# Kernel optimization log

Measured on AMD Instinct MI355X. Metric: run time of the kernel, lower is better.

The kernel has to match this reference:

```python
import jax, jax.numpy as jnp
import numpy as np

# physical constants (repo-level globals)
L1, L2, M1, M2 = 1.0, 1.0, 1.0, 1.0
G, K1 = 9.81, 0.5
A_E = 1.0   # energy-shaping stabilizer gain (a_M = 0 -> F_M term is exactly zero)
B_DAMP = 0.0
BATCH, HID = 500000, 64


def _V(q, W1, b1, W2, b2, W3, b3):
    # learned potential: [B,2] -> [B,1]
    h = jnp.tanh(q @ W1 + b1)
    h = jnp.tanh(h @ W2 + b2)
    return h @ W3 + b3


def _pot(q1, q2):
    return -G * (jnp.cos(q1 + q2) * L2 * M2 + jnp.cos(q1) * L1 * (M1 + M2)) + K1 * (0.5 * jnp.pi - q2) ** 2


def _inv_mass(q2):
    M_11 = 2 * jnp.cos(q2) * L1 * L2 * M2 + L2 ** 2 * M2 + L1 ** 2 * (M1 + M2)
    M_12 = L2 * (jnp.cos(q2) * L1 + L2) * M2
    M_22 = L2 ** 2 * M2
    DEN = M_11 * M_22 - M_12 ** 2
    return M_22 / DEN, -M_12 / DEN, M_11 / DEN


def setup_inputs() -> dict:
    key = jax.random.key(0)
    ks = jax.random.split(key, 8)
    s1 = 1.0 / np.sqrt(2.0)
    s2 = 1.0 / np.sqrt(HID)
    return {
        "x": jax.random.normal(ks[0], (BATCH, 4), jnp.float32),
        "t": jnp.zeros((1,), jnp.float32),
        "W1": jax.random.normal(ks[1], (2, HID), jnp.float32) * s1,
        "b1": jnp.zeros((HID,), jnp.float32),
        "W2": jax.random.normal(ks[2], (HID, HID), jnp.float32) * s2,
        "b2": jnp.zeros((HID,), jnp.float32),
        "W3": jax.random.normal(ks[3], (HID, 1), jnp.float32) * s2,
        "b3": jnp.zeros((1,), jnp.float32),
        "T_param": jnp.ones((1,), jnp.float32),
        "x0": jax.random.normal(ks[4], (4,), jnp.float32),
    }


def _forward(x, W1, b1, W2, b2, W3, b3, T_param, x0):
    q = x[:, :2]
    p = x[:, 2:]
    q1, q2 = q[:, 0], q[:, 1]
    p1, p2 = p[:, 0], p[:, 1]

    # u_energy_shaping = -dV/dq
    dVdq = jax.grad(lambda qq: _V(qq, W1, b1, W2, b2, W3, b3).sum())(q)
    u_es = -dVdq  # [B,2]

    # stabilizing control (a_M = 0 -> only F_E term)
    iM11, iM12, iM22 = _inv_mass(q2)
    quad = iM11 * p1 ** 2 + 2 * iM12 * p1 * p2 + iM22 * p2 ** 2  # p^T M^{-1} p
    kin = 0.5 * quad
    E = _pot(q1, q2) + kin + _V(q, W1, b1, W2, b2, W3, b3)[:, 0]

    # desired energy from x0 (set in _set_control_parameters)
    q0 = x0[:2][None, :]
    p0 = x0[2:]
    i011, i012, i022 = _inv_mass(q0[:, 1])
    kin0 = 0.5 * (i011 * p0[0] ** 2 + 2 * i012 * p0[0] * p0[1] + i022 * p0[1] ** 2)
    E_des = (_pot(q0[:, 0], q0[:, 1]) + kin0 + _V(q0, W1, b1, W2, b2, W3, b3)[:, 0])[0]

    pnorm = jnp.sqrt(quad)
    safe = jnp.where(pnorm > 0, pnorm, 1.0)
    p_hat = jnp.where((pnorm > 0)[:, None], p / safe[:, None], p)
    u_st = A_E * (E_des - E)[:, None] * p_hat

    u = u_es + u_st
    u1, u2 = u[:, 0], u[:, 1]

    # dynamics
    cq2, sq2 = jnp.cos(q2), jnp.sin(q2)
    DET = L1 ** 2 * L2 ** 2 * M2 ** 2 * (-(cq2 ** 2)) + L1 ** 2 * L2 ** 2 * M2 ** 2 + L1 ** 2 * L2 ** 2 * M1 * M2
    dq1dt = L2 ** 2 * M2 * p1 / DET - L2 * M2 * p2 * (L1 * cq2 + L2) / DET
    dq2dt = p2 * (2 * L2 * L1 * M2 * cq2 + L1 ** 2 * (M1 + M2) + L2 ** 2 * M2) / DET - L2 * M2 * p1 * (L1 * cq2 + L2) / DET
    dp1dt = -G * (jnp.sin(q1 + q2) * L2 * M2 + jnp.sin(q1) * L1 * (M1 + M2)) + u1 - B_DAMP * dq1dt
    denom = L1 ** 2 * L2 ** 2 * (M1 + sq2 ** 2 * M2) ** 2
    inner = (-(p2 ** 2) * sq2 * (cq2 * L1 + L2) * (cq2 * L2 * M2 + L1 * (M1 + M2))
             + 0.5 * p1 * p2 * sq2 * L2 * (4 * cq2 * L2 * M2 + L1 * (2 * M1 + (3 + jnp.cos(2 * q2)) * M2))
             + L2 ** 2 * (-cq2 * p1 ** 2 * sq2 * M2
                          + L1 ** 2 * (M1 + sq2 ** 2 * M2) ** 2 * (G * jnp.sin(q1 + q2) * L2 * M2 - K1 * (jnp.pi - 2 * q2))))
    dp2dt = -(inner / denom) + u2 - B_DAMP * dq2dt

    dxdt = jnp.stack([dq1dt, dq2dt, dp1dt, dp2dt], axis=1)
    return jnp.abs(T_param[0]) * dxdt


def reference(x, t, W1, b1, W2, b2, W3, b3, T_param, x0):
    # t is unused by the forward math (autonomous dynamics under ODE-solver interface)
    return _forward(x, W1, b1, W2, b2, W3, b3, T_param, x0)
```

## Files before the change

kernel.cpp:

```cpp
#include <hip/hip_runtime.h>
#include <math.h>

#define HID 64

typedef __attribute__((ext_vector_type(4))) float f32x4;
typedef __attribute__((ext_vector_type(8))) __bf16 bf16x8;
typedef __attribute__((ext_vector_type(4))) __bf16 bf16x4;

__device__ __forceinline__ float fast_tanh(float x) {
    float e = __expf(2.0f * x);
    return 1.0f - 2.0f * __builtin_amdgcn_rcpf(e + 1.0f);
}

__global__ void prep_kernel(const float* __restrict__ W1, const float* __restrict__ b1,
                            const float* __restrict__ W2, const float* __restrict__ b2,
                            const float* __restrict__ W3, const float* __restrict__ b3,
                            const float* __restrict__ x0, float* __restrict__ edes_out,
                            __bf16* __restrict__ W2bf, __bf16* __restrict__ W2Tbf) {
    int tid = threadIdx.x;
    for (int idx = tid; idx < HID * HID; idx += 256) {
        W2bf[idx] = (__bf16)W2[idx];
        int r = idx >> 6, c = idx & 63;
        W2Tbf[idx] = (__bf16)W2[c * HID + r];
    }
    if (tid < 64) {
        int j = tid;
        float q1 = x0[0], q2 = x0[1], p1 = x0[2], p2 = x0[3];
        float h1j = fast_tanh(fmaf(q1, W1[j], fmaf(q2, W1[HID + j], b1[j])));
        float z = b2[j];
#pragma unroll 1
        for (int i = 0; i < HID; i++) {
            float hi = __shfl(h1j, i, 64);
            z = fmaf(hi, W2[i * HID + j], z);
        }
        float h2 = fast_tanh(z);
        float v = h2 * W3[j];
#pragma unroll
        for (int off = 32; off; off >>= 1) v += __shfl_xor(v, off, 64);
        if (j == 0) {
            float V = v + b3[0];
            float s, c;
            __sincosf(q2, &s, &c);
            float DEN = 2.0f - c * c;
            float rDEN = __builtin_amdgcn_rcpf(DEN);
            float quad = (p1 * p1 - 2.0f * (c + 1.0f) * p1 * p2 + (2.0f * c + 3.0f) * p2 * p2) * rDEN;
            float kin = 0.5f * quad;
            float s1, c1;
            __sincosf(q1, &s1, &c1);
            float c12 = c1 * c - s1 * s;
            float dq = 1.57079632679489662f - q2;
            float pot = -9.81f * (c12 + 2.0f * c1) + 0.5f * dq * dq;
            edes_out[0] = pot + kin + V;
        }
    }
}

#define TANH8M(F, M, Q1v, Q2v)                                                                        \
    {                                                                                                 \
        float h;                                                                                      \
        h = fast_tanh(fmaf(Q1v, wa0.x, fmaf(Q2v, wb0.x, bb0.x))); F[0] = (__bf16)h; M[0] = (__bf16)fmaf(-h, h, 1.0f); \
        h = fast_tanh(fmaf(Q1v, wa0.y, fmaf(Q2v, wb0.y, bb0.y))); F[1] = (__bf16)h; M[1] = (__bf16)fmaf(-h, h, 1.0f); \
        h = fast_tanh(fmaf(Q1v, wa0.z, fmaf(Q2v, wb0.z, bb0.z))); F[2] = (__bf16)h; M[2] = (__bf16)fmaf(-h, h, 1.0f); \
        h = fast_tanh(fmaf(Q1v, wa0.w, fmaf(Q2v, wb0.w, bb0.w))); F[3] = (__bf16)h; M[3] = (__bf16)fmaf(-h, h, 1.0f); \
        h = fast_tanh(fmaf(Q1v, wa1.x, fmaf(Q2v, wb1.x, bb1.x))); F[4] = (__bf16)h; M[4] = (__bf16)fmaf(-h, h, 1.0f); \
        h = fast_tanh(fmaf(Q1v, wa1.y, fmaf(Q2v, wb1.y, bb1.y))); F[5] = (__bf16)h; M[5] = (__bf16)fmaf(-h, h, 1.0f); \
        h = fast_tanh(fmaf(Q1v, wa1.z, fmaf(Q2v, wb1.z, bb1.z))); F[6] = (__bf16)h; M[6] = (__bf16)fmaf(-h, h, 1.0f); \
        h = fast_tanh(fmaf(Q1v, wa1.w, fmaf(Q2v, wb1.w, bb1.w))); F[7] = (__bf16)h; M[7] = (__bf16)fmaf(-h, h, 1.0f); \
    }

#define L1HALF4(FA, FB, FC, FD, K0)                                         \
    do {                                                                    \
        const float4 wa0 = *(const float4*)(W1 + (K0));                     \
        const float4 wa1 = *(const float4*)(W1 + (K0) + 4);                 \
        const float4 wb0 = *(const float4*)(W1 + HID + (K0));               \
        const float4 wb1 = *(const float4*)(W1 + HID + (K0) + 4);           \
        const float4 bb0 = *(const float4*)(b1 + (K0));                     \
        const float4 bb1 = *(const float4*)(b1 + (K0) + 4);                 \
        bf16x8 mA, mB, mC, mD;                                              \
        TANH8M(FA, mA, q1A, q2A)                                            \
        TANH8M(FB, mB, q1B, q2B)                                            \
        TANH8M(FC, mC, q1C, q2C)                                            \
        TANH8M(FD, mD, q1D, q2D)                                            \
        const int mo = rowbase + ((K0) ^ swz);                              \
        *(bf16x8*)(mkA + mo) = mA;                                          \
        *(bf16x8*)(mkB + mo) = mB;                                          \
        *(bf16x8*)(mkC + mo) = mC;                                          \
        *(bf16x8*)(mkD + mo) = mD;                                          \
    } while (0)

#define MFMA __builtin_amdgcn_mfma_f32_16x16x32_bf16

#define H2ONE(Z, VP, GBUF, MT)                                                      \
    do {                                                                            \
        float h, g0_, g1_, g2_, g3_;                                                \
        h = fast_tanh(Z[0]); VP = fmaf(h, w3v.x, VP); g0_ = w3v.x * (1.0f - h * h); \
        h = fast_tanh(Z[1]); VP = fmaf(h, w3v.y, VP); g1_ = w3v.y * (1.0f - h * h); \
        h = fast_tanh(Z[2]); VP = fmaf(h, w3v.z, VP); g2_ = w3v.z * (1.0f - h * h); \
        h = fast_tanh(Z[3]); VP = fmaf(h, w3v.w, VP); g3_ = w3v.w * (1.0f - h * h); \
        bf16x4 gv = {(__bf16)g0_, (__bf16)g1_, (__bf16)g2_, (__bf16)g3_};           \
        *(bf16x4*)((GBUF) + rowbase + ((16 * (MT) + 4 * hi) ^ swz)) = gv;           \
    } while (0)

#define FWDMT(MT)                                                           \
    do {                                                                    \
        const float4 b2v = *(const float4*)(b2 + 16 * (MT) + 4 * hi);       \
        f32x4 zA = {b2v.x, b2v.y, b2v.z, b2v.w};                            \
        f32x4 zB = zA, zC = zA, zD = zA;                                    \
        const bf16x8 wf0 = *(const bf16x8*)(w2t + (MT) * 1024);             \
        zA = MFMA(wf0, a10A, zA, 0, 0, 0);                                  \
        zB = MFMA(wf0, a10B, zB, 0, 0, 0);                                  \
        zC = MFMA(wf0, a10C, zC, 0, 0, 0);                                  \
        zD = MFMA(wf0, a10D, zD, 0, 0, 0);                                  \
        const bf16x8 wf1 = *(const bf16x8*)(w2t + (MT) * 1024 + 32);        \
        zA = MFMA(wf1, a11A, zA, 0, 0, 0);                                  \
        zB = MFMA(wf1, a11B, zB, 0, 0, 0);                                  \
        zC = MFMA(wf1, a11C, zC, 0, 0, 0);                                  \
        zD = MFMA(wf1, a11D, zD, 0, 0, 0);                                  \
        const float4 w3v = *(const float4*)(W3 + 16 * (MT) + 4 * hi);       \
        H2ONE(zA, vpA, g2A, MT);                                            \
        H2ONE(zB, vpB, g2B, MT);                                            \
        H2ONE(zC, vpC, g2C, MT);                                            \
        H2ONE(zD, vpD, g2D, MT);                                            \
    } while (0)

#define DVONE(R, MK, MT, D1, D2)                                                              \
    do {                                                                                      \
        const bf16x4 mv = *(const bf16x4*)((MK) + rowbase + ((16 * (MT) + 4 * hi) ^ swz));    \
        float gi;                                                                             \
        gi = (float)mv[0] * R[0]; D1 = fmaf(w1av.x, gi, D1); D2 = fmaf(w1bv.x, gi, D2);       \
        gi = (float)mv[1] * R[1]; D1 = fmaf(w1av.y, gi, D1); D2 = fmaf(w1bv.y, gi, D2);       \
        gi = (float)mv[2] * R[2]; D1 = fmaf(w1av.z, gi, D1); D2 = fmaf(w1bv.z, gi, D2);       \
        gi = (float)mv[3] * R[3]; D1 = fmaf(w1av.w, gi, D1); D2 = fmaf(w1bv.w, gi, D2);       \
    } while (0)

#define BWDMT(MT)                                                           \
    do {                                                                    \
        f32x4 rA = {0.f, 0.f, 0.f, 0.f};                                    \
        f32x4 rB = rA, rC = rA, rD = rA;                                    \
        const bf16x8 wf0 = *(const bf16x8*)(w2b + (MT) * 1024);             \
        rA = MFMA(wf0, a20A, rA, 0, 0, 0);                                  \
        rB = MFMA(wf0, a20B, rB, 0, 0, 0);                                  \
        rC = MFMA(wf0, a20C, rC, 0, 0, 0);                                  \
        rD = MFMA(wf0, a20D, rD, 0, 0, 0);                                  \
        const bf16x8 wf1 = *(const bf16x8*)(w2b + (MT) * 1024 + 32);        \
        rA = MFMA(wf1, a21A, rA, 0, 0, 0);                                  \
        rB = MFMA(wf1, a21B, rB, 0, 0, 0);                                  \
        rC = MFMA(wf1, a21C, rC, 0, 0, 0);                                  \
        rD = MFMA(wf1, a21D, rD, 0, 0, 0);                                  \
        const float4 w1av = *(const float4*)(W1 + 16 * (MT) + 4 * hi);      \
        const float4 w1bv = *(const float4*)(W1 + HID + 16 * (MT) + 4 * hi);\
        DVONE(rA, mkA, MT, d1A, d2A);                                       \
        DVONE(rB, mkB, MT, d1B, d2B);                                       \
        DVONE(rC, mkC, MT, d1C, d2C);                                       \
        DVONE(rD, mkD, MT, d1D, d2D);                                       \
    } while (0)

#define RED2(V) V += __shfl_xor(V, 16, 64); V += __shfl_xor(V, 32, 64);

#define SEL4(A, B, C, D) ((hi == 0) ? (A) : (hi == 1) ? (B) : (hi == 2) ? (C) : (D))

__global__ __launch_bounds__(256, 2) void pend_kernel(
    const float4* __restrict__ x,
    const float* __restrict__ W1, const float* __restrict__ b1,
    const __bf16* __restrict__ W2bf, const __bf16* __restrict__ W2Tbf,
    const float* __restrict__ b2,
    const float* __restrict__ W3, const float* __restrict__ b3,
    const float* __restrict__ Tp, const float* __restrict__ edes_p,
    float4* __restrict__ out, int n)
{
    __shared__ __align__(16) __bf16 lds[4 * 8192];
    const int tid = threadIdx.x;
    const int w = tid >> 6, l = tid & 63;
    const int lo = l & 15, hi = l >> 4;
    __bf16* g2A = lds + w * 8192;
    __bf16* g2B = g2A + 1024;
    __bf16* g2C = g2B + 1024;
    __bf16* g2D = g2C + 1024;
    __bf16* mkA = g2D + 1024;
    __bf16* mkB = mkA + 1024;
    __bf16* mkC = mkB + 1024;
    __bf16* mkD = mkC + 1024;

    const float E_des = edes_p[0];
    const float Tabs = fabsf(Tp[0]);
    const float b3c = b3[0];

    const int base = blockIdx.x * 256 + w * 64;
    int eA = base + lo;       if (eA >= n) eA = n - 1;
    int eB = base + 16 + lo;  if (eB >= n) eB = n - 1;
    int eC = base + 32 + lo;  if (eC >= n) eC = n - 1;
    int eD = base + 48 + lo;  if (eD >= n) eD = n - 1;
    const float4 xvA = x[eA];
    const float4 xvB = x[eB];
    const float4 xvC = x[eC];
    const float4 xvD = x[eD];
    const float q1A = xvA.x, q2A = xvA.y, p1A = xvA.z, p2A = xvA.w;
    const float q1B = xvB.x, q2B = xvB.y, p1B = xvB.z, p2B = xvB.w;
    const float q1C = xvC.x, q2C = xvC.y, p1C = xvC.z, p2C = xvC.w;
    const float q1D = xvD.x, q2D = xvD.y, p1D = xvD.z, p2D = xvD.w;

    const int swz = (lo & 7) << 3;
    const int rowbase = lo * HID;

    bf16x8 a10A, a11A, a10B, a11B, a10C, a11C, a10D, a11D;
    L1HALF4(a10A, a10B, a10C, a10D, 8 * hi);
    L1HALF4(a11A, a11B, a11C, a11D, 32 + 8 * hi);

    const __bf16* w2t = W2Tbf + lo * HID + 8 * hi;
    const __bf16* w2b = W2bf  + lo * HID + 8 * hi;

    float vpA = 0.0f, vpB = 0.0f, vpC = 0.0f, vpD = 0.0f;
    FWDMT(0);
    FWDMT(1);
    FWDMT(2);
    FWDMT(3);

    const bf16x8 a20A = *(const bf16x8*)(g2A + rowbase + ((8 * hi) ^ swz));
    const bf16x8 a21A = *(const bf16x8*)(g2A + rowbase + ((32 + 8 * hi) ^ swz));
    const bf16x8 a20B = *(const bf16x8*)(g2B + rowbase + ((8 * hi) ^ swz));
    const bf16x8 a21B = *(const bf16x8*)(g2B + rowbase + ((32 + 8 * hi) ^ swz));
    const bf16x8 a20C = *(const bf16x8*)(g2C + rowbase + ((8 * hi) ^ swz));
    const bf16x8 a21C = *(const bf16x8*)(g2C + rowbase + ((32 + 8 * hi) ^ swz));
    const bf16x8 a20D = *(const bf16x8*)(g2D + rowbase + ((8 * hi) ^ swz));
    const bf16x8 a21D = *(const bf16x8*)(g2D + rowbase + ((32 + 8 * hi) ^ swz));

    float d1A = 0.f, d2A = 0.f, d1B = 0.f, d2B = 0.f;
    float d1C = 0.f, d2C = 0.f, d1D = 0.f, d2D = 0.f;
    BWDMT(0);
    BWDMT(1);
    BWDMT(2);
    BWDMT(3);

    RED2(vpA) RED2(vpB) RED2(vpC) RED2(vpD)
    RED2(d1A) RED2(d1B) RED2(d1C) RED2(d1D)
    RED2(d2A) RED2(d2B) RED2(d2C) RED2(d2D)

    const float V    = SEL4(vpA, vpB, vpC, vpD) + b3c;
    const float dVq1 = SEL4(d1A, d1B, d1C, d1D);
    const float dVq2 = SEL4(d2A, d2B, d2C, d2D);
    const float q1 = SEL4(q1A, q1B, q1C, q1D);
    const float q2 = SEL4(q2A, q2B, q2C, q2D);
    const float p1 = SEL4(p1A, p1B, p1C, p1D);
    const float p2 = SEL4(p2A, p2B, p2C, p2D);

    float s2q, c2q, s1q, c1q;
    __sincosf(q2, &s2q, &c2q);
    __sincosf(q1, &s1q, &c1q);
    const float s12 = s1q * c2q + c1q * s2q;
    const float c12 = c1q * c2q - s1q * s2q;

    const float cc = c2q, s = s2q;
    const float DEN = 2.0f - cc * cc;
    const float rDEN = __builtin_amdgcn_rcpf(DEN);
    const float cp1 = cc + 1.0f;

    const float quad = (p1 * p1 - 2.0f * cp1 * p1 * p2 + (2.0f * cc + 3.0f) * p2 * p2) * rDEN;
    const float kin = 0.5f * quad;
    const float dqa = 1.57079632679489662f - q2;
    const float pot = -9.81f * (c12 + 2.0f * c1q) + 0.5f * dqa * dqa;
    const float E = pot + kin + V;

    const float fac = (quad > 0.0f) ? __builtin_amdgcn_rsqf(quad) : 1.0f;
    const float coef = E_des - E;
    const float u1 = -dVq1 + coef * p1 * fac;
    const float u2 = -dVq2 + coef * p2 * fac;

    const float dq1dt = (p1 - cp1 * p2) * rDEN;
    const float dq2dt = ((2.0f * cc + 3.0f) * p2 - cp1 * p1) * rDEN;
    const float dp1dt = -9.81f * (s12 + 2.0f * s1q) + u1;

    const float inner = -p2 * p2 * s * cp1 * (cc + 2.0f)
                + p1 * p2 * s * (fmaf(cc, cc, fmaf(2.0f, cc, 2.0f)))
                - cc * p1 * p1 * s
                + DEN * DEN * (fmaf(9.81f, s12, -0.5f * (3.14159265358979324f - 2.0f * q2)));
    const float dp2dt = -(inner * rDEN * rDEN) + u2;

    const int row = base + l;
    if (row < n) {
        float4 o;
        o.x = Tabs * dq1dt;
        o.y = Tabs * dq2dt;
        o.z = Tabs * dp1dt;
        o.w = Tabs * dp2dt;
        out[row] = o;
    }
}

extern "C" void kernel_launch(void* const* d_in, const int* in_sizes, int n_in,
                              void* d_out, int out_size, void* d_ws, size_t ws_size,
                              hipStream_t stream) {
    const float* x  = (const float*)d_in[0];
    const float* W1 = (const float*)d_in[2];
    const float* b1 = (const float*)d_in[3];
    const float* W2 = (const float*)d_in[4];
    const float* b2 = (const float*)d_in[5];
    const float* W3 = (const float*)d_in[6];
    const float* b3 = (const float*)d_in[7];
    const float* Tp = (const float*)d_in[8];
    const float* x0 = (const float*)d_in[9];

    float* ws = (float*)d_ws;
    float* edes = ws;
    __bf16* W2bf  = (__bf16*)(ws + 16);
    __bf16* W2Tbf = W2bf + HID * HID;

    prep_kernel<<<1, 256, 0, stream>>>(W1, b1, W2, b2, W3, b3, x0, edes, W2bf, W2Tbf);

    int n = in_sizes[0] / 4;
    int blocks = (n + 255) / 256;
    pend_kernel<<<blocks, 256, 0, stream>>>((const float4*)x, W1, b1, W2bf, W2Tbf,
                                            b2, W3, b3, Tp, edes, (float4*)d_out, n);
}
```

Measured before the change: 44.48 us.

## Process sub-tiles in two sequential pairs to halve LDS and raise occupancy

Instead of running the MLP forward and backward for all four 16-row sub-tiles at once, each wave now handles two sub-tiles, then the other two, reusing half-sized LDS scratch buffers. This halves per-block LDS and cuts live registers, which lets launch bounds rise from 2 to 4 blocks per CU for more latency hiding. In exchange there is less instruction-level parallelism per wave and an added block-wide barrier between the two pairs. The per-wave buffers may only need a wave-level barrier.

Measured after the change: 103.7 us. 2.33x slower.

```diff
diff --git a/kernel.cpp b/kernel.cpp
--- a/kernel.cpp
+++ b/kernel.cpp
@@ -68,7 +68,7 @@
         h = fast_tanh(fmaf(Q1v, wa1.w, fmaf(Q2v, wb1.w, bb1.w))); F[7] = (__bf16)h; M[7] = (__bf16)fmaf(-h, h, 1.0f); \
     }
 
-#define L1HALF4(FA, FB, FC, FD, K0)                                         \
+#define L1HB(FX, FY, K0, Q1a_, Q2a_, Q1b_, Q2b_)                            \
     do {                                                                    \
         const float4 wa0 = *(const float4*)(W1 + (K0));                     \
         const float4 wa1 = *(const float4*)(W1 + (K0) + 4);                 \
@@ -76,16 +76,12 @@
         const float4 wb1 = *(const float4*)(W1 + HID + (K0) + 4);           \
         const float4 bb0 = *(const float4*)(b1 + (K0));                     \
         const float4 bb1 = *(const float4*)(b1 + (K0) + 4);                 \
-        bf16x8 mA, mB, mC, mD;                                              \
-        TANH8M(FA, mA, q1A, q2A)                                            \
-        TANH8M(FB, mB, q1B, q2B)                                            \
-        TANH8M(FC, mC, q1C, q2C)                                            \
-        TANH8M(FD, mD, q1D, q2D)                                            \
+        bf16x8 mX_, mY_;                                                    \
+        TANH8M(FX, mX_, Q1a_, Q2a_)                                         \
+        TANH8M(FY, mY_, Q1b_, Q2b_)                                         \
         const int mo = rowbase + ((K0) ^ swz);                              \
-        *(bf16x8*)(mkA + mo) = mA;                                          \
-        *(bf16x8*)(mkB + mo) = mB;                                          \
-        *(bf16x8*)(mkC + mo) = mC;                                          \
-        *(bf16x8*)(mkD + mo) = mD;                                          \
+        *(bf16x8*)(mk0 + mo) = mX_;                                         \
+        *(bf16x8*)(mk1 + mo) = mY_;                                         \
     } while (0)
 
 #define MFMA __builtin_amdgcn_mfma_f32_16x16x32_bf16
@@ -101,26 +97,20 @@
         *(bf16x4*)((GBUF) + rowbase + ((16 * (MT) + 4 * hi) ^ swz)) = gv;           \
     } while (0)
 
-#define FWDMT(MT)                                                           \
+#define FWDMT2(MT, VPa_, VPb_)                                              \
     do {                                                                    \
         const float4 b2v = *(const float4*)(b2 + 16 * (MT) + 4 * hi);       \
-        f32x4 zA = {b2v.x, b2v.y, b2v.z, b2v.w};                            \
-        f32x4 zB = zA, zC = zA, zD = zA;                                    \
+        f32x4 zX = {b2v.x, b2v.y, b2v.z, b2v.w};                            \
+        f32x4 zY = zX;                                                      \
         const bf16x8 wf0 = *(const bf16x8*)(w2t + (MT) * 1024);             \
-        zA = MFMA(wf0, a10A, zA, 0, 0, 0);                                  \
-        zB = MFMA(wf0, a10B, zB, 0, 0, 0);                                  \
-        zC = MFMA(wf0, a10C, zC, 0, 0, 0);                                  \
-        zD = MFMA(wf0, a10D, zD, 0, 0, 0);                                  \
+        zX = MFMA(wf0, a10X, zX, 0, 0, 0);                                  \
+        zY = MFMA(wf0, a10Y, zY, 0, 0, 0);                                  \
         const bf16x8 wf1 = *(const bf16x8*)(w2t + (MT) * 1024 + 32);        \
-        zA = MFMA(wf1, a11A, zA, 0, 0, 0);                                  \
-        zB = MFMA(wf1, a11B, zB, 0, 0, 0);                                  \
-        zC = MFMA(wf1, a11C, zC, 0, 0, 0);                                  \
-        zD = MFMA(wf1, a11D, zD, 0, 0, 0);                                  \
+        zX = MFMA(wf1, a11X, zX, 0, 0, 0);                                  \
+        zY = MFMA(wf1, a11Y, zY, 0, 0, 0);                                  \
         const float4 w3v = *(const float4*)(W3 + 16 * (MT) + 4 * hi);       \
-        H2ONE(zA, vpA, g2A, MT);                                            \
-        H2ONE(zB, vpB, g2B, MT);                                            \
-        H2ONE(zC, vpC, g2C, MT);                                            \
-        H2ONE(zD, vpD, g2D, MT);                                            \
+        H2ONE(zX, VPa_, g20, MT);                                           \
+        H2ONE(zY, VPb_, g21, MT);                                           \
     } while (0)
 
 #define DVONE(R, MK, MT, D1, D2)                                                              \
@@ -133,33 +123,46 @@
         gi = (float)mv[3] * R[3]; D1 = fmaf(w1av.w, gi, D1); D2 = fmaf(w1bv.w, gi, D2);       \
     } while (0)
 
-#define BWDMT(MT)                                                           \
+#define BWDMT2(MT, D1a_, D2a_, D1b_, D2b_)                                  \
     do {                                                                    \
-        f32x4 rA = {0.f, 0.f, 0.f, 0.f};                                    \
-        f32x4 rB = rA, rC = rA, rD = rA;                                    \
+        f32x4 rX = {0.f, 0.f, 0.f, 0.f};                                    \
+        f32x4 rY = rX;                                                      \
         const bf16x8 wf0 = *(const bf16x8*)(w2b + (MT) * 1024);             \
-        rA = MFMA(wf0, a20A, rA, 0, 0, 0);                                  \
-        rB = MFMA(wf0, a20B, rB, 0, 0, 0);                                  \
-        rC = MFMA(wf0, a20C, rC, 0, 0, 0);                                  \
-        rD = MFMA(wf0, a20D, rD, 0, 0, 0);                                  \
+        rX = MFMA(wf0, a20X, rX, 0, 0, 0);                                  \
+        rY = MFMA(wf0, a20Y, rY, 0, 0, 0);                                  \
         const bf16x8 wf1 = *(const bf16x8*)(w2b + (MT) * 1024 + 32);        \
-        rA = MFMA(wf1, a21A, rA, 0, 0, 0);                                  \
-        rB = MFMA(wf1, a21B, rB, 0, 0, 0);                                  \
-        rC = MFMA(wf1, a21C, rC, 0, 0, 0);                                  \
-        rD = MFMA(wf1, a21D, rD, 0, 0, 0);                                  \
+        rX = MFMA(wf1, a21X, rX, 0, 0, 0);                                  \
+        rY = MFMA(wf1, a21Y, rY, 0, 0, 0);                                  \
         const float4 w1av = *(const float4*)(W1 + 16 * (MT) + 4 * hi);      \
         const float4 w1bv = *(const float4*)(W1 + HID + 16 * (MT) + 4 * hi);\
-        DVONE(rA, mkA, MT, d1A, d2A);                                       \
-        DVONE(rB, mkB, MT, d1B, d2B);                                       \
-        DVONE(rC, mkC, MT, d1C, d2C);                                       \
-        DVONE(rD, mkD, MT, d1D, d2D);                                       \
+        DVONE(rX, mk0, MT, D1a_, D2a_);                                     \
+        DVONE(rY, mk1, MT, D1b_, D2b_);                                     \
+    } while (0)
+
+#define DOPAIR(Q1a_, Q2a_, Q1b_, Q2b_, VPa_, VPb_, D1a_, D2a_, D1b_, D2b_)          \
+    do {                                                                            \
+        bf16x8 a10X, a11X, a10Y, a11Y;                                              \
+        L1HB(a10X, a10Y, 8 * hi, Q1a_, Q2a_, Q1b_, Q2b_);                           \
+        L1HB(a11X, a11Y, 32 + 8 * hi, Q1a_, Q2a_, Q1b_, Q2b_);                      \
+        FWDMT2(0, VPa_, VPb_);                                                      \
+        FWDMT2(1, VPa_, VPb_);                                                      \
+        FWDMT2(2, VPa_, VPb_);                                                      \
+        FWDMT2(3, VPa_, VPb_);                                                      \
+        const bf16x8 a20X = *(const bf16x8*)(g20 + rowbase + ((8 * hi) ^ swz));     \
+        const bf16x8 a21X = *(const bf16x8*)(g20 + rowbase + ((32 + 8 * hi) ^ swz));\
+        const bf16x8 a20Y = *(const bf16x8*)(g21 + rowbase + ((8 * hi) ^ swz));     \
+        const bf16x8 a21Y = *(const bf16x8*)(g21 + rowbase + ((32 + 8 * hi) ^ swz));\
+        BWDMT2(0, D1a_, D2a_, D1b_, D2b_);                                          \
+        BWDMT2(1, D1a_, D2a_, D1b_, D2b_);                                          \
+        BWDMT2(2, D1a_, D2a_, D1b_, D2b_);                                          \
+        BWDMT2(3, D1a_, D2a_, D1b_, D2b_);                                          \
     } while (0)
 
 #define RED2(V) V += __shfl_xor(V, 16, 64); V += __shfl_xor(V, 32, 64);
 
 #define SEL4(A, B, C, D) ((hi == 0) ? (A) : (hi == 1) ? (B) : (hi == 2) ? (C) : (D))
 
-__global__ __launch_bounds__(256, 2) void pend_kernel(
+__global__ __launch_bounds__(256, 4) void pend_kernel(
     const float4* __restrict__ x,
     const float* __restrict__ W1, const float* __restrict__ b1,
     const __bf16* __restrict__ W2bf, const __bf16* __restrict__ W2Tbf,
@@ -168,18 +171,14 @@
     const float* __restrict__ Tp, const float* __restrict__ edes_p,
     float4* __restrict__ out, int n)
 {
-    __shared__ __align__(16) __bf16 lds[4 * 8192];
+    __shared__ __align__(16) __bf16 lds[4 * 4096];
     const int tid = threadIdx.x;
     const int w = tid >> 6, l = tid & 63;
     const int lo = l & 15, hi = l >> 4;
-    __bf16* g2A = lds + w * 8192;
-    __bf16* g2B = g2A + 1024;
-    __bf16* g2C = g2B + 1024;
-    __bf16* g2D = g2C + 1024;
-    __bf16* mkA = g2D + 1024;
-    __bf16* mkB = mkA + 1024;
-    __bf16* mkC = mkB + 1024;
-    __bf16* mkD = mkC + 1024;
+    __bf16* g20 = lds + w * 4096;
+    __bf16* g21 = g20 + 1024;
+    __bf16* mk0 = g21 + 1024;
+    __bf16* mk1 = mk0 + 1024;
 
     const float E_des = edes_p[0];
     const float Tabs = fabsf(Tp[0]);
@@ -202,34 +201,18 @@
     const int swz = (lo & 7) << 3;
     const int rowbase = lo * HID;
 
-    bf16x8 a10A, a11A, a10B, a11B, a10C, a11C, a10D, a11D;
-    L1HALF4(a10A, a10B, a10C, a10D, 8 * hi);
-    L1HALF4(a11A, a11B, a11C, a11D, 32 + 8 * hi);
-
     const __bf16* w2t = W2Tbf + lo * HID + 8 * hi;
     const __bf16* w2b = W2bf  + lo * HID + 8 * hi;
 
     float vpA = 0.0f, vpB = 0.0f, vpC = 0.0f, vpD = 0.0f;
-    FWDMT(0);
-    FWDMT(1);
-    FWDMT(2);
-    FWDMT(3);
-
-    const bf16x8 a20A = *(const bf16x8*)(g2A + rowbase + ((8 * hi) ^ swz));
-    const bf16x8 a21A = *(const bf16x8*)(g2A + rowbase + ((32 + 8 * hi) ^ swz));
-    const bf16x8 a20B = *(const bf16x8*)(g2B + rowbase + ((8 * hi) ^ swz));
-    const bf16x8 a21B = *(const bf16x8*)(g2B + rowbase + ((32 + 8 * hi) ^ swz));
-    const bf16x8 a20C = *(const bf16x8*)(g2C + rowbase + ((8 * hi) ^ swz));
-    const bf16x8 a21C = *(const bf16x8*)(g2C + rowbase + ((32 + 8 * hi) ^ swz));
-    const bf16x8 a20D = *(const bf16x8*)(g2D + rowbase + ((8 * hi) ^ swz));
-    const bf16x8 a21D = *(const bf16x8*)(g2D + rowbase + ((32 + 8 * hi) ^ swz));
-
     float d1A = 0.f, d2A = 0.f, d1B = 0.f, d2B = 0.f;
     float d1C = 0.f, d2C = 0.f, d1D = 0.f, d2D = 0.f;
-    BWDMT(0);
-    BWDMT(1);
-    BWDMT(2);
-    BWDMT(3);
+
+    DOPAIR(q1A, q2A, q1B, q2B, vpA, vpB, d1A, d2A, d1B, d2B);
+
+    __syncthreads();
+
+    DOPAIR(q1C, q2C, q1D, q2D, vpC, vpD, d1C, d2C, d1D, d2D);
 
     RED2(vpA) RED2(vpB) RED2(vpC) RED2(vpD)
     RED2(d1A) RED2(d1B) RED2(d1C) RED2(d1D)
```
